# Optimization experiments

Measured on AMD Instinct MI355X. Metric: run time of the kernel, lower is better.

Reference implementation:

```python
import jax, jax.numpy as jnp
import numpy as np

NEG_INF = -9.0e15  # matches torch reference's -9e15 masking constant


def setup_inputs() -> dict:
    key = jax.random.key(0)
    k1, k2, k3, k4 = jax.random.split(key, 4)
    N, F_IN, F_OUT = 8192, 256, 256
    x = jax.random.normal(k1, (N, F_IN), dtype=jnp.float32)
    adj = jax.random.randint(k2, (N, N), 0, 2, dtype=jnp.int32)
    W = jax.random.normal(k3, (F_OUT, F_IN), dtype=jnp.float32) * (1.0 / np.sqrt(F_IN))
    a = jax.random.normal(k4, (2 * F_OUT,), dtype=jnp.float32) * (1.0 / np.sqrt(2 * F_OUT))
    return {"x": x, "adj": adj, "W": W, "a": a}


def reference(x, adj, W, a):
    # h = W x  -> [N, F_OUT]
    h = x @ W.T
    F_OUT = h.shape[1]
    # The concat trick: e[i, j] = leaky_relu(a1 . h_i + a2 . h_j)
    # (repeat_interleave gives h_i as the first half, repeat gives h_j as the second half)
    a1, a2 = a[:F_OUT], a[F_OUT:]
    s_i = h @ a1  # [N] -- contribution of destination/row node i
    s_j = h @ a2  # [N] -- contribution of source/col node j
    e = jax.nn.leaky_relu(s_i[:, None] + s_j[None, :], negative_slope=0.2)  # [N, N]
    att = jnp.where(adj > 0, e, jnp.asarray(NEG_INF, dtype=e.dtype))
    att = jax.nn.softmax(att, axis=1)
    # dropout is identity in eval mode / for the deterministic reference
    h_prime = att @ h  # [N, F_OUT]
    return h_prime
```

## Files before the change

### kernel.cpp

```cpp
#include <hip/hip_runtime.h>
#include <hip/hip_bf16.h>

typedef __attribute__((ext_vector_type(4))) float f32x4;
typedef __attribute__((ext_vector_type(8))) short s16x8;
typedef __attribute__((ext_vector_type(4))) int i32x4;
typedef __attribute__((ext_vector_type(4))) unsigned short u16x4;

#define NEG_INF_F (-9.0e15f)
#define LOG2E_F 1.44269504088896340736f
#define N_ROWS 8192
#define F_DIM 256

__device__ __forceinline__ unsigned short f2bf(float f) {
    unsigned int u = __builtin_bit_cast(unsigned int, f);
    u += 0x7fffu + ((u >> 16) & 1u);
    return (unsigned short)(u >> 16);
}

__device__ __forceinline__ float fast_exp2(float x) {
#if __has_builtin(__builtin_amdgcn_exp2f)
    return __builtin_amdgcn_exp2f(x);
#else
    return exp2f(x);
#endif
}

__device__ __forceinline__ short f2bf_fast(float f) {
    __hip_bfloat16 b = __float2bfloat16(f);
    return __builtin_bit_cast(short, b);
}

__global__ __launch_bounds__(256) void k0_pack(const int* __restrict__ adj,
                                               unsigned* __restrict__ mask32) {
    const int t0 = (int)blockIdx.x * 256 + (int)threadIdx.x;
    const int nt = (int)gridDim.x * 256;
#pragma unroll 1
    for (int w = t0; w < (N_ROWS * N_ROWS / 32); w += nt) {
        const int* p = adj + (size_t)w * 32;
        unsigned m = 0;
#pragma unroll
        for (int i = 0; i < 8; ++i) {
            i32x4 v = *(const i32x4*)(p + i * 4);
            m |= (v[0] > 0 ? 1u : 0u) << (i * 4);
            m |= (v[1] > 0 ? 2u : 0u) << (i * 4);
            m |= (v[2] > 0 ? 4u : 0u) << (i * 4);
            m |= (v[3] > 0 ? 8u : 0u) << (i * 4);
        }
        mask32[w] = m;
    }
}

__global__ __launch_bounds__(256) void k1_gemm(const float* __restrict__ x,
                                               const float* __restrict__ W,
                                               unsigned short* __restrict__ hTp) {
    __shared__ float xT[128][64];
    __shared__ float wT[128][64];
    const int tid = threadIdx.x;
    const int rb = blockIdx.x >> 2, fbk = blockIdx.x & 3;
    const int row0 = rb * 64, f0 = fbk * 64;
    const int rs = tid >> 2, cs = tid & 3;
    const int r0 = (tid & 15) * 4, fc = (tid >> 4) * 4;
    float acc[4][4];
#pragma unroll
    for (int i = 0; i < 4; ++i)
#pragma unroll
        for (int j = 0; j < 4; ++j) acc[i][j] = 0.0f;

#pragma unroll 1
    for (int p = 0; p < 2; ++p) {
        const int kb = p * 128;
        if (p) __syncthreads();
        const float* xrow = x + (size_t)(row0 + rs) * F_DIM + kb + cs * 32;
        const float* wrow = W + (size_t)(f0 + rs) * F_DIM + kb + cs * 32;
#pragma unroll
        for (int i = 0; i < 8; ++i) {
            f32x4 xv = *(const f32x4*)(xrow + i * 4);
            f32x4 wv = *(const f32x4*)(wrow + i * 4);
#pragma unroll
            for (int jj = 0; jj < 4; ++jj) {
                xT[cs * 32 + i * 4 + jj][rs] = xv[jj];
                wT[cs * 32 + i * 4 + jj][rs] = wv[jj];
            }
        }
        __syncthreads();
#pragma unroll 4
        for (int kk = 0; kk < 128; ++kk) {
            f32x4 xv = *(const f32x4*)&xT[kk][r0];
            f32x4 wv = *(const f32x4*)&wT[kk][fc];
#pragma unroll
            for (int i = 0; i < 4; ++i)
#pragma unroll
                for (int j = 0; j < 4; ++j)
                    acc[i][j] = fmaf(xv[i], wv[j], acc[i][j]);
        }
    }
    const int kblk = (row0 + r0) >> 3, kslot = (row0 + r0) & 7;
#pragma unroll
    for (int j = 0; j < 4; ++j) {
        u16x4 t;
        t[0] = f2bf(acc[0][j]); t[1] = f2bf(acc[1][j]);
        t[2] = f2bf(acc[2][j]); t[3] = f2bf(acc[3][j]);
        *(u16x4*)(hTp + (size_t)kblk * 2048 + (f0 + fc + j) * 8 + kslot) = t;
    }
}

__global__ __launch_bounds__(256) void kva(const float* __restrict__ W,
                                           const float* __restrict__ a,
                                           float* __restrict__ va) {
    const int k = threadIdx.x;
    const int b = blockIdx.x;
    const float* av = a + b * 256;
    float s0 = 0.f, s1 = 0.f, s2 = 0.f, s3 = 0.f;
#pragma unroll 8
    for (int f = 0; f < 256; f += 4) {
        s0 = fmaf(av[f],     W[(size_t)f * 256 + k],       s0);
        s1 = fmaf(av[f + 1], W[(size_t)(f + 1) * 256 + k], s1);
        s2 = fmaf(av[f + 2], W[(size_t)(f + 2) * 256 + k], s2);
        s3 = fmaf(av[f + 3], W[(size_t)(f + 3) * 256 + k], s3);
    }
    va[b * 256 + k] = (s0 + s1) + (s2 + s3);
}

__global__ __launch_bounds__(256) void k1b_s(const float* __restrict__ x,
                                             const float* __restrict__ va,
                                             float* __restrict__ s1,
                                             float* __restrict__ s2) {
    const int tid = threadIdx.x, lane = tid & 63, w = tid >> 6;
    f32x4 a1 = *(const f32x4*)(va + lane * 4);
    f32x4 a2 = *(const f32x4*)(va + 256 + lane * 4);
    const int row0 = blockIdx.x * 32 + w * 8;
#pragma unroll 1
    for (int rr = 0; rr < 8; ++rr) {
        const int row = row0 + rr;
        f32x4 hv = *(const f32x4*)(x + (size_t)row * F_DIM + lane * 4);
        float p1 = hv[0] * a1[0] + hv[1] * a1[1] + hv[2] * a1[2] + hv[3] * a1[3];
        float p2 = hv[0] * a2[0] + hv[1] * a2[1] + hv[2] * a2[2] + hv[3] * a2[3];
#pragma unroll
        for (int o = 32; o; o >>= 1) { p1 += __shfl_xor(p1, o); p2 += __shfl_xor(p2, o); }
        if (lane == 0) { s1[row] = p1; s2[row] = p2; }
    }
}

__global__ __launch_bounds__(256) void kmax(const unsigned* __restrict__ mask32,
                                            const float* __restrict__ s2,
                                            float* __restrict__ Mrow) {
    __shared__ float s2l[8192];
    const int tid = threadIdx.x, lane = tid & 63, wv = tid >> 6;
#pragma unroll
    for (int i = 0; i < 8; ++i) {
        const int idx = (i * 256 + tid) * 4;
        *(f32x4*)&s2l[idx] = *(const f32x4*)(s2 + idx);
    }
    __syncthreads();
    const int row = (int)blockIdx.x * 4 + wv;
    const unsigned* __restrict__ mr = mask32 + (size_t)row * 256;
    float vmax = NEG_INF_F;
#pragma unroll 1
    for (int wi = 0; wi < 4; ++wi) {
        const unsigned m = mr[lane * 4 + wi];
        const int kb = (lane * 4 + wi) * 32;
#pragma unroll
        for (int cc = 0; cc < 8; ++cc) {
            const int c = (cc + lane) & 7;
            f32x4 v = *(const f32x4*)&s2l[kb + c * 4];
            const unsigned sh = (unsigned)(c * 4);
            vmax = fmaxf(vmax, ((m >> (sh + 0)) & 1u) ? v[0] : NEG_INF_F);
            vmax = fmaxf(vmax, ((m >> (sh + 1)) & 1u) ? v[1] : NEG_INF_F);
            vmax = fmaxf(vmax, ((m >> (sh + 2)) & 1u) ? v[2] : NEG_INF_F);
            vmax = fmaxf(vmax, ((m >> (sh + 3)) & 1u) ? v[3] : NEG_INF_F);
        }
    }
#pragma unroll
    for (int o = 32; o; o >>= 1) vmax = fmaxf(vmax, __shfl_xor(vmax, o));
    if (lane == 0) Mrow[row] = vmax;
}


#define P_ONE(D, SV, BIT, SI, MC)                                             \
    { float t_ = (SI) + (SV); t_ = fmaxf(t_, 0.2f * t_);                      \
      D = fast_exp2(fmaf(((bb_ & (BIT)) ? t_ : NEG_INF_F), LOG2E_F, -(MC))); }

#define RG_STEP(ACC, ACCL, BFR, MW, SI, MC)                                   \
    {                                                                         \
        const unsigned bb_ = ((MW) >> koff) & 0xffu;                          \
        float p0_, p1_, p2_, p3_, p4_, p5_, p6_, p7_;                         \
        P_ONE(p0_, svA_[0], 1u, SI, MC)   P_ONE(p1_, svA_[1], 2u, SI, MC)     \
        P_ONE(p2_, svA_[2], 4u, SI, MC)   P_ONE(p3_, svA_[3], 8u, SI, MC)     \
        P_ONE(p4_, svB_[0], 16u, SI, MC)  P_ONE(p5_, svB_[1], 32u, SI, MC)    \
        P_ONE(p6_, svB_[2], 64u, SI, MC)  P_ONE(p7_, svB_[3], 128u, SI, MC)   \
        s16x8 af_;                                                            \
        af_[0] = f2bf_fast(p0_); af_[1] = f2bf_fast(p1_);                     \
        af_[2] = f2bf_fast(p2_); af_[3] = f2bf_fast(p3_);                     \
        af_[4] = f2bf_fast(p4_); af_[5] = f2bf_fast(p5_);                     \
        af_[6] = f2bf_fast(p6_); af_[7] = f2bf_fast(p7_);                     \
        _Pragma("unroll")                                                     \
        for (int nt_ = 0; nt_ < 8; ++nt_)                                     \
            ACC[nt_] = __builtin_amdgcn_mfma_f32_16x16x32_bf16(af_, BFR[nt_], ACC[nt_], 0, 0, 0); \
        ACCL = __builtin_amdgcn_mfma_f32_16x16x32_bf16(af_, bones, ACCL, 0, 0, 0); \
    }

#define HALF_STEP(BFR, MWA, MWB, K)                                           \
    {                                                                         \
        const f32x4 svA_ = *(const f32x4*)(s2 + (K) + koff);                  \
        const f32x4 svB_ = *(const f32x4*)(s2 + (K) + koff + 4);              \
        RG_STEP(accA, accLA, BFR, MWA, siA, mCA)                              \
        RG_STEP(accB, accLB, BFR, MWB, siB, mCB)                              \
    }

#define LOAD_B(DST, K)                                                        \
    _Pragma("unroll")                                                         \
    for (int nt_ = 0; nt_ < 8; ++nt_)                                         \
        DST[nt_] = *(const s16x8*)(hTp + (unsigned)(((K) >> 3) + kg) * 2048u + vb + (unsigned)(nt_ * 128));

__global__ __launch_bounds__(256) void k2_attn(const unsigned* __restrict__ mask32,
                                               const unsigned short* __restrict__ hTp,
                                               const float* __restrict__ s1,
                                               const float* __restrict__ s2,
                                               const float* __restrict__ Mrow,
                                               float* __restrict__ out) {
    __shared__ float lbuf[4][2][16];
    __shared__ float accbuf[3][16][132];

    const int tid = threadIdx.x;
    const int lane = tid & 63;
    const int wc = tid >> 6;
    const int lane15 = lane & 15, kg = lane >> 4, koff = kg * 8;
    const int rowblk = (int)blockIdx.x >> 1;
    const int fh = (int)blockIdx.x & 1;
    const int row0 = rowblk * 32;
    const int mrowA = row0 + lane15, mrowB = row0 + 16 + lane15;
    const int fb = fh * 128;
    const int kbase = wc * 2048;
    const float siA = s1[mrowA], siB = s1[mrowB];
    const float tmxA = siA + Mrow[mrowA], tmxB = siB + Mrow[mrowB];
    const float mCA = fmaxf(tmxA, 0.2f * tmxA) * LOG2E_F;
    const float mCB = fmaxf(tmxB, 0.2f * tmxB) * LOG2E_F;
    const unsigned* __restrict__ mA32 = mask32 + (size_t)mrowA * 256;
    const unsigned* __restrict__ mB32 = mask32 + (size_t)mrowB * 256;

    f32x4 accA[8], accB[8], accLA, accLB;
#pragma unroll
    for (int nt = 0; nt < 8; ++nt) {
        f32x4 z = {0.f, 0.f, 0.f, 0.f};
        accA[nt] = z; accB[nt] = z;
    }
    { f32x4 z = {0.f, 0.f, 0.f, 0.f}; accLA = z; accLB = z; }

    s16x8 bones;
#pragma unroll
    for (int j = 0; j < 8; ++j) bones[j] = (short)0x3F80;

    const unsigned vb = (unsigned)(fb + lane15) * 8u;

    s16x8 bA[8], bB[8];
    LOAD_B(bA, kbase)
    unsigned mwA = mA32[kbase >> 5], mwB = mB32[kbase >> 5];

#pragma unroll 1
    for (int it = 0; it < 64; it += 2) {
        const int k0 = kbase + it * 32;
        const int k1 = k0 + 32;
        const int k2n = (it + 2 < 64) ? (k0 + 64) : kbase;

        LOAD_B(bB, k1)
        const unsigned mwnA = mA32[k1 >> 5], mwnB = mB32[k1 >> 5];

        HALF_STEP(bA, mwA, mwB, k0);

        LOAD_B(bA, k2n)
        mwA = mA32[k2n >> 5]; mwB = mB32[k2n >> 5];

        HALF_STEP(bB, mwnA, mwnB, k1);
    }

    if (lane15 == 0) {
#pragma unroll
        for (int r = 0; r < 4; ++r) {
            lbuf[wc][0][kg * 4 + r] = accLA[r];
            lbuf[wc][1][kg * 4 + r] = accLB[r];
        }
    }

    if (wc > 0) {
#pragma unroll
        for (int r = 0; r < 4; ++r)
#pragma unroll
            for (int nt = 0; nt < 8; ++nt)
                accbuf[wc - 1][kg * 4 + r][nt * 16 + lane15] = accA[nt][r];
    }
    __syncthreads();
    if (wc == 0) {
#pragma unroll
        for (int r = 0; r < 4; ++r) {
            const int dr = kg * 4 + r;
            const float lt = (lbuf[0][0][dr] + lbuf[1][0][dr]) + (lbuf[2][0][dr] + lbuf[3][0][dr]);
            const float inv = 1.0f / lt;
            float* orow_p = out + (size_t)(row0 + dr) * F_DIM + fb + lane15;
#pragma unroll
            for (int nt = 0; nt < 8; ++nt) {
                const float v = accA[nt][r] + accbuf[0][dr][nt * 16 + lane15]
                              + accbuf[1][dr][nt * 16 + lane15]
                              + accbuf[2][dr][nt * 16 + lane15];
                orow_p[nt * 16] = v * inv;
            }
        }
    }
    __syncthreads();

    if (wc > 0) {
#pragma unroll
        for (int r = 0; r < 4; ++r)
#pragma unroll
            for (int nt = 0; nt < 8; ++nt)
                accbuf[wc - 1][kg * 4 + r][nt * 16 + lane15] = accB[nt][r];
    }
    __syncthreads();
    if (wc == 0) {
#pragma unroll
        for (int r = 0; r < 4; ++r) {
            const int dr = kg * 4 + r;
            const float lt = (lbuf[0][1][dr] + lbuf[1][1][dr]) + (lbuf[2][1][dr] + lbuf[3][1][dr]);
            const float inv = 1.0f / lt;
            float* orow_p = out + (size_t)(row0 + 16 + dr) * F_DIM + fb + lane15;
#pragma unroll
            for (int nt = 0; nt < 8; ++nt) {
                const float v = accB[nt][r] + accbuf[0][dr][nt * 16 + lane15]
                              + accbuf[1][dr][nt * 16 + lane15]
                              + accbuf[2][dr][nt * 16 + lane15];
                orow_p[nt * 16] = v * inv;
            }
        }
    }
}

extern "C" void kernel_launch(void* const* d_in, const int* in_sizes, int n_in,
                              void* d_out, int out_size, void* d_ws, size_t ws_size,
                              hipStream_t stream) {
    (void)in_sizes; (void)n_in; (void)out_size; (void)ws_size;
    const float* x  = (const float*)d_in[0];
    const int*  adj = (const int*)d_in[1];
    const float* W  = (const float*)d_in[2];
    const float* a  = (const float*)d_in[3];
    float* out = (float*)d_out;
    char* ws = (char*)d_ws;
    unsigned short* hTp = (unsigned short*)ws;
    float* s1 = (float*)(ws + (4 << 20));
    float* s2 = (float*)(ws + (4 << 20) + (32 << 10));
    float* va = (float*)(ws + (4 << 20) + (64 << 10));
    float* Mr = (float*)(ws + (4 << 20) + (96 << 10));
    unsigned* mk = (unsigned*)(ws + (4 << 20) + (128 << 10));

    k0_pack<<<2048, 256, 0, stream>>>(adj, mk);
    k1_gemm<<<512, 256, 0, stream>>>(x, W, hTp);
    kva<<<2, 256, 0, stream>>>(W, a, va);
    k1b_s<<<256, 256, 0, stream>>>(x, va, s1, s2);
    kmax<<<2048, 256, 0, stream>>>(mk, s2, Mr);
    k2_attn<<<512, 256, 0, stream>>>(mk, hTp, s1, s2, Mr, out);
}
```

Baseline: 180.1 us.

## Merge prep kernels into one launch, ballot-pack mask, deepen attention prefetch, XCD-aware mapping

```diff
diff --git a/kernel.cpp b/kernel.cpp
--- a/kernel.cpp
+++ b/kernel.cpp
@@ -30,114 +30,117 @@
     return __builtin_bit_cast(short, b);
 }
 
-__global__ __launch_bounds__(256) void k0_pack(const int* __restrict__ adj,
-                                               unsigned* __restrict__ mask32) {
-    const int t0 = (int)blockIdx.x * 256 + (int)threadIdx.x;
-    const int nt = (int)gridDim.x * 256;
-#pragma unroll 1
-    for (int w = t0; w < (N_ROWS * N_ROWS / 32); w += nt) {
-        const int* p = adj + (size_t)w * 32;
-        unsigned m = 0;
-#pragma unroll
-        for (int i = 0; i < 8; ++i) {
-            i32x4 v = *(const i32x4*)(p + i * 4);
-            m |= (v[0] > 0 ? 1u : 0u) << (i * 4);
-            m |= (v[1] > 0 ? 2u : 0u) << (i * 4);
-            m |= (v[2] > 0 ? 4u : 0u) << (i * 4);
-            m |= (v[3] > 0 ? 8u : 0u) << (i * 4);
-        }
-        mask32[w] = m;
-    }
-}
-
-__global__ __launch_bounds__(256) void k1_gemm(const float* __restrict__ x,
-                                               const float* __restrict__ W,
-                                               unsigned short* __restrict__ hTp) {
+__global__ __launch_bounds__(256) void k01(const float* __restrict__ x,
+                                           const float* __restrict__ W,
+                                           unsigned short* __restrict__ hTp,
+                                           const float* __restrict__ a,
+                                           const int* __restrict__ adj,
+                                           unsigned long long* __restrict__ mask,
+                                           float* __restrict__ s1,
+                                           float* __restrict__ s2) {
     __shared__ float xT[128][64];
     __shared__ float wT[128][64];
+    const int bb = (int)blockIdx.x;
     const int tid = threadIdx.x;
-    const int rb = blockIdx.x >> 2, fbk = blockIdx.x & 3;
-    const int row0 = rb * 64, f0 = fbk * 64;
-    const int rs = tid >> 2, cs = tid & 3;
-    const int r0 = (tid & 15) * 4, fc = (tid >> 4) * 4;
-    float acc[4][4];
-#pragma unroll
-    for (int i = 0; i < 4; ++i)
-#pragma unroll
-        for (int j = 0; j < 4; ++j) acc[i][j] = 0.0f;
-
-#pragma unroll 1
-    for (int p = 0; p < 2; ++p) {
-        const int kb = p * 128;
-        if (p) __syncthreads();
-        const float* xrow = x + (size_t)(row0 + rs) * F_DIM + kb + cs * 32;
-        const float* wrow = W + (size_t)(f0 + rs) * F_DIM + kb + cs * 32;
-#pragma unroll
-        for (int i = 0; i < 8; ++i) {
-            f32x4 xv = *(const f32x4*)(xrow + i * 4);
-            f32x4 wv = *(const f32x4*)(wrow + i * 4);
-#pragma unroll
-            for (int jj = 0; jj < 4; ++jj) {
-                xT[cs * 32 + i * 4 + jj][rs] = xv[jj];
-                wT[cs * 32 + i * 4 + jj][rs] = wv[jj];
-            }
+
+    if (bb < 512) {
+        const int rb = bb >> 2, fbk = bb & 3;
+        const int row0 = rb * 64, f0 = fbk * 64;
+        const int rs = tid >> 2, cs = tid & 3;
+        const int r0 = (tid & 15) * 4, fc = (tid >> 4) * 4;
+        float acc[4][4];
+#pragma unroll
+        for (int i = 0; i < 4; ++i)
+#pragma unroll
+            for (int j = 0; j < 4; ++j) acc[i][j] = 0.0f;
+
+#pragma unroll 1
+        for (int p = 0; p < 2; ++p) {
+            const int kb = p * 128;
+            if (p) __syncthreads();
+            const float* xrow = x + (size_t)(row0 + rs) * F_DIM + kb + cs * 32;
+            const float* wrow = W + (size_t)(f0 + rs) * F_DIM + kb + cs * 32;
+#pragma unroll
+            for (int i = 0; i < 8; ++i) {
+                f32x4 xv = *(const f32x4*)(xrow + i * 4);
+                f32x4 wv = *(const f32x4*)(wrow + i * 4);
+#pragma unroll
+                for (int jj = 0; jj < 4; ++jj) {
+                    xT[cs * 32 + i * 4 + jj][rs] = xv[jj];
+                    wT[cs * 32 + i * 4 + jj][rs] = wv[jj];
+                }
+            }
+            __syncthreads();
+#pragma unroll 4
+            for (int kk = 0; kk < 128; ++kk) {
+                f32x4 xv = *(const f32x4*)&xT[kk][r0];
+                f32x4 wv = *(const f32x4*)&wT[kk][fc];
+#pragma unroll
+                for (int i = 0; i < 4; ++i)
+#pragma unroll
+                    for (int j = 0; j < 4; ++j)
+                        acc[i][j] = fmaf(xv[i], wv[j], acc[i][j]);
+            }
+        }
+        const int kblk = (row0 + r0) >> 3, kslot = (row0 + r0) & 7;
+#pragma unroll
+        for (int j = 0; j < 4; ++j) {
+            u16x4 t;
+            t[0] = f2bf(acc[0][j]); t[1] = f2bf(acc[1][j]);
+            t[2] = f2bf(acc[2][j]); t[3] = f2bf(acc[3][j]);
+            *(u16x4*)(hTp + (size_t)kblk * 2048 + (f0 + fc + j) * 8 + kslot) = t;
+        }
+    } else if (bb < 768) {
+        float* va = &xT[0][0];
+        {
+            const int k = tid;
+            const float* a1p = a;
+            const float* a2p = a + 256;
+            float u0 = 0.f, u1 = 0.f, v0 = 0.f, v1 = 0.f;
+#pragma unroll 8
+            for (int f = 0; f < 256; f += 2) {
+                const float w0 = W[(size_t)f * 256 + k];
+                const float w1 = W[(size_t)(f + 1) * 256 + k];
+                u0 = fmaf(a1p[f], w0, u0);  u1 = fmaf(a1p[f + 1], w1, u1);
+                v0 = fmaf(a2p[f], w0, v0);  v1 = fmaf(a2p[f + 1], w1, v1);
+            }
+            va[k] = u0 + u1;
+            va[256 + k] = v0 + v1;
         }
         __syncthreads();
-#pragma unroll 4
-        for (int kk = 0; kk < 128; ++kk) {
-            f32x4 xv = *(const f32x4*)&xT[kk][r0];
-            f32x4 wv = *(const f32x4*)&wT[kk][fc];
-#pragma unroll
-            for (int i = 0; i < 4; ++i)
-#pragma unroll
-                for (int j = 0; j < 4; ++j)
-                    acc[i][j] = fmaf(xv[i], wv[j], acc[i][j]);
-        }
-    }
-    const int kblk = (row0 + r0) >> 3, kslot = (row0 + r0) & 7;
-#pragma unroll
-    for (int j = 0; j < 4; ++j) {
-        u16x4 t;
-        t[0] = f2bf(acc[0][j]); t[1] = f2bf(acc[1][j]);
-        t[2] = f2bf(acc[2][j]); t[3] = f2bf(acc[3][j]);
-        *(u16x4*)(hTp + (size_t)kblk * 2048 + (f0 + fc + j) * 8 + kslot) = t;
-    }
-}
-
-__global__ __launch_bounds__(256) void kva(const float* __restrict__ W,
-                                           const float* __restrict__ a,
-                                           float* __restrict__ va) {
-    const int k = threadIdx.x;
-    const int b = blockIdx.x;
-    const float* av = a + b * 256;
-    float s0 = 0.f, s1 = 0.f, s2 = 0.f, s3 = 0.f;
-#pragma unroll 8
-    for (int f = 0; f < 256; f += 4) {
-        s0 = fmaf(av[f],     W[(size_t)f * 256 + k],       s0);
-        s1 = fmaf(av[f + 1], W[(size_t)(f + 1) * 256 + k], s1);
-        s2 = fmaf(av[f + 2], W[(size_t)(f + 2) * 256 + k], s2);
-        s3 = fmaf(av[f + 3], W[(size_t)(f + 3) * 256 + k], s3);
-    }
-    va[b * 256 + k] = (s0 + s1) + (s2 + s3);
-}
-
-__global__ __launch_bounds__(256) void k1b_s(const float* __restrict__ x,
-                                             const float* __restrict__ va,
-                                             float* __restrict__ s1,
-                                             float* __restrict__ s2) {
-    const int tid = threadIdx.x, lane = tid & 63, w = tid >> 6;
-    f32x4 a1 = *(const f32x4*)(va + lane * 4);
-    f32x4 a2 = *(const f32x4*)(va + 256 + lane * 4);
-    const int row0 = blockIdx.x * 32 + w * 8;
-#pragma unroll 1
-    for (int rr = 0; rr < 8; ++rr) {
-        const int row = row0 + rr;
-        f32x4 hv = *(const f32x4*)(x + (size_t)row * F_DIM + lane * 4);
-        float p1 = hv[0] * a1[0] + hv[1] * a1[1] + hv[2] * a1[2] + hv[3] * a1[3];
-        float p2 = hv[0] * a2[0] + hv[1] * a2[1] + hv[2] * a2[2] + hv[3] * a2[3];
-#pragma unroll
-        for (int o = 32; o; o >>= 1) { p1 += __shfl_xor(p1, o); p2 += __shfl_xor(p2, o); }
-        if (lane == 0) { s1[row] = p1; s2[row] = p2; }
+        const int lane = tid & 63, w = tid >> 6;
+        f32x4 a1 = *(const f32x4*)(va + lane * 4);
+        f32x4 a2 = *(const f32x4*)(va + 256 + lane * 4);
+        const int row0 = (bb - 512) * 32 + w * 8;
+#pragma unroll 1
+        for (int rr = 0; rr < 8; ++rr) {
+            const int row = row0 + rr;
+            f32x4 hv = *(const f32x4*)(x + (size_t)row * F_DIM + lane * 4);
+            float p1 = hv[0] * a1[0] + hv[1] * a1[1] + hv[2] * a1[2] + hv[3] * a1[3];
+            float p2 = hv[0] * a2[0] + hv[1] * a2[1] + hv[2] * a2[2] + hv[3] * a2[3];
+#pragma unroll
+            for (int o = 32; o; o >>= 1) { p1 += __shfl_xor(p1, o); p2 += __shfl_xor(p2, o); }
+            if (lane == 0) { s1[row] = p1; s2[row] = p2; }
+        }
+    } else {
+        const int lane = tid & 63;
+        const int gw = ((bb - 768) * 256 + tid) >> 6;
+        const int nw = (3840 * 256) >> 6;
+#pragma unroll 1
+        for (int w4 = gw * 4; w4 < (N_ROWS * N_ROWS / 64); w4 += nw * 4) {
+            const size_t base = (size_t)w4 * 64 + lane;
+            const int v0 = adj[base];
+            const int v1 = adj[base + 64];
+            const int v2 = adj[base + 128];
+            const int v3 = adj[base + 192];
+            const unsigned long long b0 = __ballot(v0 > 0);
+            const unsigned long long b1 = __ballot(v1 > 0);
+            const unsigned long long b2 = __ballot(v2 > 0);
+            const unsigned long long b3 = __ballot(v3 > 0);
+            if (lane == 0) {
+                mask[w4] = b0; mask[w4 + 1] = b1; mask[w4 + 2] = b2; mask[w4 + 3] = b3;
+            }
+        }
     }
 }
 
@@ -199,18 +202,24 @@
         ACCL = __builtin_amdgcn_mfma_f32_16x16x32_bf16(af_, bones, ACCL, 0, 0, 0); \
     }
 
-#define HALF_STEP(BFR, MWA, MWB, K)                                           \
+#define STEP4(BFR, T)                                                         \
     {                                                                         \
-        const f32x4 svA_ = *(const f32x4*)(s2 + (K) + koff);                  \
-        const f32x4 svB_ = *(const f32x4*)(s2 + (K) + koff + 4);              \
-        RG_STEP(accA, accLA, BFR, MWA, siA, mCA)                              \
-        RG_STEP(accB, accLB, BFR, MWB, siB, mCB)                              \
-    }
-
-#define LOAD_B(DST, K)                                                        \
-    _Pragma("unroll")                                                         \
-    for (int nt_ = 0; nt_ < 8; ++nt_)                                         \
-        DST[nt_] = *(const s16x8*)(hTp + (unsigned)(((K) >> 3) + kg) * 2048u + vb + (unsigned)(nt_ * 128));
+        const int k0_ = kbase + (T) * 32;                                     \
+        const unsigned mwA_ = mA32[k0_ >> 5];                                 \
+        const unsigned mwB_ = mB32[k0_ >> 5];                                 \
+        const f32x4 svA_ = *(const f32x4*)(s2 + k0_ + koff);                  \
+        const f32x4 svB_ = *(const f32x4*)(s2 + k0_ + koff + 4);              \
+        RG_STEP(accA, accLA, BFR, mwA_, siA, mCA)                             \
+        RG_STEP(accB, accLB, BFR, mwB_, siB, mCB)                             \
+    }
+
+#define LOAD_B(DST, T)                                                        \
+    {                                                                         \
+        const int kt_ = kbase + (T) * 32;                                     \
+        _Pragma("unroll")                                                     \
+        for (int nt_ = 0; nt_ < 8; ++nt_)                                     \
+            DST[nt_] = *(const s16x8*)(hTp + (unsigned)((kt_ >> 3) + kg) * 2048u + vb + (unsigned)(nt_ * 128)); \
+    }
 
 __global__ __launch_bounds__(256) void k2_attn(const unsigned* __restrict__ mask32,
                                                const unsigned short* __restrict__ hTp,
@@ -225,8 +234,10 @@
     const int lane = tid & 63;
     const int wc = tid >> 6;
     const int lane15 = lane & 15, kg = lane >> 4, koff = kg * 8;
-    const int rowblk = (int)blockIdx.x >> 1;
-    const int fh = (int)blockIdx.x & 1;
+    const int b = (int)blockIdx.x;
+    const int xcd = b & 7;
+    const int fh = xcd >> 2;
+    const int rowblk = (b >> 3) * 4 + (xcd & 3);
     const int row0 = rowblk * 32;
     const int mrowA = row0 + lane15, mrowB = row0 + 16 + lane15;
     const int fb = fh * 128;
@@ -252,25 +263,15 @@
 
     const unsigned vb = (unsigned)(fb + lane15) * 8u;
 
-    s16x8 bA[8], bB[8];
-    LOAD_B(bA, kbase)
-    unsigned mwA = mA32[kbase >> 5], mwB = mB32[kbase >> 5];
-
-#pragma unroll 1
-    for (int it = 0; it < 64; it += 2) {
-        const int k0 = kbase + it * 32;
-        const int k1 = k0 + 32;
-        const int k2n = (it + 2 < 64) ? (k0 + 64) : kbase;
-
-        LOAD_B(bB, k1)
-        const unsigned mwnA = mA32[k1 >> 5], mwnB = mB32[k1 >> 5];
-
-        HALF_STEP(bA, mwA, mwB, k0);
-
-        LOAD_B(bA, k2n)
-        mwA = mA32[k2n >> 5]; mwB = mB32[k2n >> 5];
-
-        HALF_STEP(bB, mwnA, mwnB, k1);
+    s16x8 b0[8], b1[8], b2[8], b3[8];
+    LOAD_B(b0, 0) LOAD_B(b1, 1) LOAD_B(b2, 2) LOAD_B(b3, 3)
+
+#pragma unroll 1
+    for (int it = 0; it < 64; it += 4) {
+        STEP4(b0, it)     LOAD_B(b0, (it + 4) & 63)
+        STEP4(b1, it + 1) LOAD_B(b1, (it + 5) & 63)
+        STEP4(b2, it + 2) LOAD_B(b2, (it + 6) & 63)
+        STEP4(b3, it + 3) LOAD_B(b3, (it + 7) & 63)
     }
 
     if (lane15 == 0) {
@@ -346,14 +347,10 @@
     unsigned short* hTp = (unsigned short*)ws;
     float* s1 = (float*)(ws + (4 << 20));
     float* s2 = (float*)(ws + (4 << 20) + (32 << 10));
-    float* va = (float*)(ws + (4 << 20) + (64 << 10));
     float* Mr = (float*)(ws + (4 << 20) + (96 << 10));
-    unsigned* mk = (unsigned*)(ws + (4 << 20) + (128 << 10));
-
-    k0_pack<<<2048, 256, 0, stream>>>(adj, mk);
-    k1_gemm<<<512, 256, 0, stream>>>(x, W, hTp);
-    kva<<<2, 256, 0, stream>>>(W, a, va);
-    k1b_s<<<256, 256, 0, stream>>>(x, va, s1, s2);
-    kmax<<<2048, 256, 0, stream>>>(mk, s2, Mr);
-    k2_attn<<<512, 256, 0, stream>>>(mk, hTp, s1, s2, Mr, out);
-}
+    unsigned long long* mk = (unsigned long long*)(ws + (4 << 20) + (128 << 10));
+
+    k01<<<4608, 256, 0, stream>>>(x, W, hTp, a, adj, mk, s1, s2);
+    kmax<<<2048, 256, 0, stream>>>((const unsigned*)mk, s2, Mr);
+    k2_attn<<<512, 256, 0, stream>>>((const unsigned*)mk, hTp, s1, s2, Mr, out);
+}
```

Result: slower. 229.5 us (+27.4%).
